# Kernel tuning notes

Measured on AMD Instinct MI355X. Metric: run time of the kernel, lower is better.

The kernel has to match this reference:

```python
import jax, jax.numpy as jnp
import numpy as np

B, S, T = 128, 512, 128
E, He, Ed, H = 512, 512, 512, 512


def setup_inputs() -> dict:
    key = jax.random.key(0)
    ks = jax.random.split(key, 13)
    w = lambda k, shape: jax.random.normal(k, shape, jnp.float32) * 0.02
    return {
        "trg_embed": jax.random.normal(ks[0], (B, T, E), jnp.float32),
        "edit_representation_final": jax.random.normal(ks[1], (1, B, 2 * Ed), jnp.float32),
        "edit_representation_cell_state": jax.random.normal(ks[2], (1, B, 2 * Ed), jnp.float32),
        "encoder_hidden": jax.random.normal(ks[3], (B, S, 2 * He), jnp.float32),
        "encoder_final": jax.random.normal(ks[4], (1, B, 2 * He), jnp.float32),
        "encoder_cell_state": jax.random.normal(ks[5], (1, B, 2 * He), jnp.float32),
        "src_mask": jnp.ones((B, 1, S), dtype=bool),
        "W_key": w(ks[6], (2 * He, H)),
        "W_query": w(ks[7], (H, H)),
        "w_energy": w(ks[8], (H,)),
        "W_bridge": w(ks[9], (2 * He + 2 * Ed, H)),
        "b_bridge": jnp.zeros((H,), jnp.float32),
        "W_ih": w(ks[10], (4 * H, E + 2 * He + 2 * Ed)),
        "W_hh": w(ks[11], (4 * H, H)),
        "b_ih": jnp.zeros((4 * H,), jnp.float32),
        "b_hh": jnp.zeros((4 * H,), jnp.float32),
        "W_pre": w(ks[12], (H, H + 2 * He + E)),
    }


def reference(trg_embed, edit_representation_final, edit_representation_cell_state,
              encoder_hidden, encoder_final, encoder_cell_state, src_mask,
              W_key, W_query, w_energy, W_bridge, b_bridge,
              W_ih, W_hh, b_ih, b_hh, W_pre):
    # bridge: init hidden / cell from final encoder + edit states  [1,B,H]
    h0 = jnp.tanh(jnp.concatenate([encoder_final, edit_representation_final], -1) @ W_bridge + b_bridge)
    c0 = jnp.tanh(jnp.concatenate([encoder_cell_state, edit_representation_cell_state], -1) @ W_bridge + b_bridge)
    proj_key = encoder_hidden @ W_key              # [B,S,H] (computed once)
    edit_flat = edit_representation_final[0]       # [B,2*Ed]
    mask = src_mask[:, 0, :]                       # [B,S]
    bias = b_ih + b_hh

    def step(carry, x_t):
        h, c = carry                               # [B,H] each
        # Bahdanau attention
        q = h @ W_query                            # [B,H]
        scores = jnp.tanh(q[:, None, :] + proj_key) @ w_energy   # [B,S]
        scores = jnp.where(mask, scores, -jnp.inf)
        alphas = jax.nn.softmax(scores, axis=-1)
        context = jnp.einsum('bs,bsd->bd', alphas, encoder_hidden)  # [B,2*He]
        # LSTM cell (torch gate order: i, f, g, o)
        rnn_in = jnp.concatenate([x_t, context, edit_flat], -1)
        gates = rnn_in @ W_ih.T + h @ W_hh.T + bias
        i_g, f_g, g_g, o_g = jnp.split(gates, 4, axis=-1)
        c_new = jax.nn.sigmoid(f_g) * c + jax.nn.sigmoid(i_g) * jnp.tanh(g_g)
        h_new = jax.nn.sigmoid(o_g) * jnp.tanh(c_new)
        # pre-output projection (dropout in eval mode = identity)
        pre = jnp.concatenate([x_t, h_new, context], -1) @ W_pre.T
        return (h_new, c_new), (h_new, pre)

    (h_last, c_last), (states, pre_outs) = jax.lax.scan(
        step, (h0[0], c0[0]), jnp.swapaxes(trg_embed, 0, 1))
    decoder_states = jnp.swapaxes(states, 0, 1)       # [B,T,H]
    pre_output_vectors = jnp.swapaxes(pre_outs, 0, 1) # [B,T,H]
    return decoder_states, h_last[None], pre_output_vectors
```

## Files before the change

### kernel.cpp

```cpp
#include <hip/hip_runtime.h>
#include <hip/hip_bf16.h>

typedef unsigned short u16;
typedef unsigned int u32;
typedef unsigned char u8;

typedef __attribute__((ext_vector_type(8))) __bf16 bf16x8;
typedef __attribute__((ext_vector_type(4))) float f32x4;
typedef __attribute__((ext_vector_type(2))) float f32x2;

__device__ __forceinline__ float fast_tanh(float x){
    float e = __expf(2.0f*x);
    return 1.0f - 2.0f/(e+1.0f);
}
__device__ __forceinline__ float fast_sigmoid(float x){
    return 1.0f/(1.0f+__expf(-x));
}
__device__ __forceinline__ float bflo(u32 u){ return __uint_as_float(u<<16); }
__device__ __forceinline__ float bfhi(u32 u){ return __uint_as_float(u & 0xffff0000u); }
__device__ __forceinline__ float bf2f(u16 u){ return __uint_as_float(((u32)u)<<16); }
__device__ __forceinline__ u16 f2bf(float v){
    __hip_bfloat16 h = __float2bfloat16(v);
    return *reinterpret_cast<u16*>(&h);
}
__device__ __forceinline__ f32x2 fp8lo(u32 u){ return __builtin_amdgcn_cvt_pk_f32_fp8(u, false); }
__device__ __forceinline__ f32x2 fp8hi(u32 u){ return __builtin_amdgcn_cvt_pk_f32_fp8(u, true); }

__device__ __forceinline__ void gridbar(int* bar, int e){
    __syncthreads();
    if (threadIdx.x == 0){
        const int g = blockIdx.x & 7;
        int* gcnt = bar + g*32;
        int* gall = bar + 256;
        int* gate = bar + 288;
        int prev = __hip_atomic_fetch_add(gcnt, 1, __ATOMIC_ACQ_REL, __HIP_MEMORY_SCOPE_AGENT);
        if (prev == e*32 - 1){
            int pg = __hip_atomic_fetch_add(gall, 1, __ATOMIC_ACQ_REL, __HIP_MEMORY_SCOPE_AGENT);
            if (pg == e*8 - 1)
                __hip_atomic_store(gate, e, __ATOMIC_RELEASE, __HIP_MEMORY_SCOPE_AGENT);
        }
        while (__hip_atomic_load(gate, __ATOMIC_RELAXED, __HIP_MEMORY_SCOPE_AGENT) < e)
            __builtin_amdgcn_s_sleep(4);
        (void)__hip_atomic_load(gate, __ATOMIC_ACQUIRE, __HIP_MEMORY_SCOPE_AGENT);
    }
    __syncthreads();
}

__device__ __forceinline__ void pairbar(int* pflags, int e){
    __syncthreads();
    if (threadIdx.x == 0){
        __hip_atomic_store(&pflags[blockIdx.x*32], e, __ATOMIC_RELEASE, __HIP_MEMORY_SCOPE_AGENT);
        int partner = (blockIdx.x ^ 1)*32;
        while (__hip_atomic_load(&pflags[partner], __ATOMIC_RELAXED, __HIP_MEMORY_SCOPE_AGENT) < e)
            __builtin_amdgcn_s_sleep(2);
        (void)__hip_atomic_load(&pflags[partner], __ATOMIC_ACQUIRE, __HIP_MEMORY_SCOPE_AGENT);
    }
    __syncthreads();
}

template<int C_MODE, int HAS_BIAS>
__global__ __launch_bounds__(256) void mfma_gemm(
    const u16* __restrict__ A, int lda,
    const u16* __restrict__ Bw, int ldb,
    const float* __restrict__ bias,
    void* __restrict__ Cp, long ldc, int K)
{
    __shared__ u16 Ash[128*64];
    __shared__ u16 Bsh[128*64];
    const int tid  = threadIdx.x;
    const int w    = tid >> 6;
    const int lane = tid & 63;
    const int wr   = w >> 1, wc = w & 1;
    const int row0 = blockIdx.y * 128, col0 = blockIdx.x * 128;

    f32x4 acc[4][4];
    #pragma unroll
    for (int i = 0; i < 4; i++)
        #pragma unroll
        for (int j = 0; j < 4; j++)
            acc[i][j] = f32x4{0.f,0.f,0.f,0.f};

    for (int k0 = 0; k0 < K; k0 += 64) {
        #pragma unroll
        for (int it = 0; it < 4; it++) {
            int j = it*256 + tid;
            int row = j >> 3, s = j & 7;
            const u16* src = A + (size_t)(row0 + row) * lda + k0 + ((s ^ (row & 7)) << 3);
            __builtin_amdgcn_global_load_lds(
                (const __attribute__((address_space(1))) unsigned int*)src,
                (__attribute__((address_space(3))) unsigned int*)(Ash + (size_t)(it*256 + w*64)*8),
                16, 0, 0);
        }
        #pragma unroll
        for (int it = 0; it < 4; it++) {
            int j = it*256 + tid;
            int row = j >> 3, s = j & 7;
            const u16* src = Bw + (size_t)(col0 + row) * ldb + k0 + ((s ^ (row & 7)) << 3);
            __builtin_amdgcn_global_load_lds(
                (const __attribute__((address_space(1))) unsigned int*)src,
                (__attribute__((address_space(3))) unsigned int*)(Bsh + (size_t)(it*256 + w*64)*8),
                16, 0, 0);
        }
        __syncthreads();
        #pragma unroll
        for (int kh = 0; kh < 2; kh++) {
            bf16x8 af[4], bg[4];
            #pragma unroll
            for (int f = 0; f < 4; f++) {
                int row = wr*64 + f*16 + (lane & 15);
                int slot = (kh*4 + (lane >> 4)) ^ (row & 7);
                af[f] = *(const bf16x8*)(Ash + row*64 + slot*8);
                int nn = wc*64 + f*16 + (lane & 15);
                int slot2 = (kh*4 + (lane >> 4)) ^ (nn & 7);
                bg[f] = *(const bf16x8*)(Bsh + nn*64 + slot2*8);
            }
            #pragma unroll
            for (int fm = 0; fm < 4; fm++)
                #pragma unroll
                for (int fn = 0; fn < 4; fn++)
                    acc[fm][fn] = __builtin_amdgcn_mfma_f32_16x16x32_bf16(af[fm], bg[fn], acc[fm][fn], 0, 0, 0);
        }
        __syncthreads();
    }

    #pragma unroll
    for (int fm = 0; fm < 4; fm++) {
        #pragma unroll
        for (int fn = 0; fn < 4; fn++) {
            int col = col0 + wc*64 + fn*16 + (lane & 15);
            #pragma unroll
            for (int r = 0; r < 4; r++) {
                int row = row0 + wr*64 + fm*16 + ((lane >> 4)<<2) + r;
                float v = acc[fm][fn][r];
                if (HAS_BIAS) v += bias[col];
                if (C_MODE == 1)
                    ((u16*)Cp)[(size_t)row * ldc + col] = f2bf(v);
                else
                    ((float*)Cp)[(((size_t)(row & 127)) << 16) + ((size_t)(row >> 7) << 9) + col] = v;
            }
        }
    }
}

__global__ __launch_bounds__(1024, 4) void k_mega(
    u16* __restrict__ pre_in,
    const u16* __restrict__ Wq_t,
    const u8*  __restrict__ pk8,
    const float* __restrict__ we_g,
    const u8*  __restrict__ enc8,
    const u16* __restrict__ Wg,
    const u16* __restrict__ edit_part,
    u16* __restrict__ gates_part,
    float* __restrict__ scores_g,
    u16* __restrict__ h_glob,
    float* __restrict__ cbuf,
    float* __restrict__ out_states,
    float* __restrict__ out_hlast,
    int* __restrict__ bar)
{
    __shared__ __align__(16) u8 pk_lds[131072];
    __shared__ __align__(16) u8 scr[24576];
    __shared__ float hs[512];
    __shared__ float qf[544];
    __shared__ float al[512];
    float* qp   = (float*)scr;
    float* red  = (float*)scr;
    float* spp  = (float*)scr;
    float* cp8  = (float*)scr;
    float* fold = (float*)(scr + 18432);
    u16* Ash = (u16*)scr;
    u16* Bsh = (u16*)(scr + 16384);
    int* pflags = bar + 320;
    const int bid = blockIdx.x, tid = threadIdx.x;
    const int w = tid >> 6, lane = tid & 63;
    const int b = bid >> 1, half = bid & 1;

    {
        const u8* srcb = pk8 + ((size_t)(b*512 + half*256))*512;
        #pragma unroll
        for (int i = 0; i < 8; i++)
            __builtin_amdgcn_global_load_lds(
                (const __attribute__((address_space(1))) unsigned int*)(srcb + i*16384 + tid*16),
                (__attribute__((address_space(3))) unsigned int*)(pk_lds + i*16384 + (size_t)w*1024),
                16, 0, 0);
    }
    float wel[16];
    {
        const int l = lane & 31;
        #pragma unroll
        for (int i = 0; i < 16; i++) wel[i] = we_g[l*16 + i];
    }
    asm volatile("s_waitcnt vmcnt(0)" ::: "memory");
    __syncthreads();

    for (int t = 0; t < 129; t++) {
        if (t == 0) {
            if (tid < 512) hs[tid] = bf2f(h_glob[b*512 + tid]);
        } else if (tid < 512) {
            const int j = tid;
            float g4[4];
            #pragma unroll
            for (int g = 0; g < 4; g++) {
                float s = bf2f(edit_part[b*2048 + g*512 + j]);
                #pragma unroll
                for (int kk = 0; kk < 8; kk++)
                    s += bf2f(gates_part[(size_t)kk*262144 + b*2048 + g*512 + j]);
                g4[g] = s;
            }
            float c  = cbuf[(size_t)(t & 1)*65536 + b*512 + j];
            float cn = fast_sigmoid(g4[1])*c + fast_sigmoid(g4[0])*fast_tanh(g4[2]);
            float hn = fast_sigmoid(g4[3])*fast_tanh(cn);
            cbuf[(size_t)((t+1) & 1)*65536 + b*512 + j] = cn;
            hs[j] = hn;
            u16 hb = f2bf(hn);
            h_glob[b*512 + j] = hb;
            pre_in[(size_t)(t-1)*262144 + b*2048 + 1536 + j] = hb;
            out_states[(size_t)b*65536 + (size_t)(t-1)*512 + j] = hn;
            if (t == 128) out_hlast[b*512 + j] = hn;
        }
        if (t == 128) break;
        __syncthreads();
        {
            const int j = tid & 511, kh3 = tid >> 9;
            const uint4* row = (const uint4*)(Wq_t + (size_t)j*512 + (size_t)kh3*256);
            float a = 0.f;
            #pragma unroll 8
            for (int c8 = 0; c8 < 32; c8++) {
                uint4 u = row[c8];
                int k = kh3*256 + c8*8;
                a += hs[k+0]*bflo(u.x) + hs[k+1]*bfhi(u.x)
                   + hs[k+2]*bflo(u.y) + hs[k+3]*bfhi(u.y)
                   + hs[k+4]*bflo(u.z) + hs[k+5]*bfhi(u.z)
                   + hs[k+6]*bflo(u.w) + hs[k+7]*bfhi(u.w);
            }
            qp[tid] = a;
        }
        __syncthreads();
        if (tid < 512) qf[tid + (tid >> 4)] = qp[tid] + qp[512 + tid];
        __syncthreads();
        {
            float ql[16];
            const int l = lane & 31;
            #pragma unroll
            for (int i = 0; i < 16; i++) ql[i] = qf[l*17 + i];
            #pragma unroll
            for (int it = 0; it < 8; it++) {
                const int s = it*32 + w*2 + (lane >> 5);
                const uint4 u = *(const uint4*)(pk_lds + (size_t)s*512 + l*16);
                float a2 = 0.f;
                f32x2 p;
                p = fp8lo(u.x); a2 += fast_tanh(ql[0]+p.x)*wel[0] + fast_tanh(ql[1]+p.y)*wel[1];
                p = fp8hi(u.x); a2 += fast_tanh(ql[2]+p.x)*wel[2] + fast_tanh(ql[3]+p.y)*wel[3];
                p = fp8lo(u.y); a2 += fast_tanh(ql[4]+p.x)*wel[4] + fast_tanh(ql[5]+p.y)*wel[5];
                p = fp8hi(u.y); a2 += fast_tanh(ql[6]+p.x)*wel[6] + fast_tanh(ql[7]+p.y)*wel[7];
                p = fp8lo(u.z); a2 += fast_tanh(ql[8]+p.x)*wel[8] + fast_tanh(ql[9]+p.y)*wel[9];
                p = fp8hi(u.z); a2 += fast_tanh(ql[10]+p.x)*wel[10] + fast_tanh(ql[11]+p.y)*wel[11];
                p = fp8lo(u.w); a2 += fast_tanh(ql[12]+p.x)*wel[12] + fast_tanh(ql[13]+p.y)*wel[13];
                p = fp8hi(u.w); a2 += fast_tanh(ql[14]+p.x)*wel[14] + fast_tanh(ql[15]+p.y)*wel[15];
                #pragma unroll
                for (int o = 16; o; o >>= 1) a2 += __shfl_xor(a2, o);
                if (l == 0) spp[s] = a2;
            }
        }
        __syncthreads();
        if (tid < 256) scores_g[b*512 + half*256 + tid] = spp[tid];
        pairbar(pflags, t + 1);

        {
            const int s = tid & 511;
            float sc = scores_g[b*512 + s];
            float m = sc;
            #pragma unroll
            for (int o = 32; o; o >>= 1) m = fmaxf(m, __shfl_xor(m, o));
            if (lane == 0) red[w] = m;
            __syncthreads();
            m = red[0];
            #pragma unroll
            for (int i = 1; i < 16; i++) m = fmaxf(m, red[i]);
            float p = __expf(sc - m);
            float sm = p;
            #pragma unroll
            for (int o = 32; o; o >>= 1) sm += __shfl_xor(sm, o);
            if (lane == 0) red[16 + w] = sm;
            __syncthreads();
            sm = red[16];
            #pragma unroll
            for (int i = 17; i < 24; i++) sm += red[i];
            al[s] = p * (1.f / sm);
        }
        __syncthreads();
        {
            const int ch = tid & 31, sg = tid >> 5;
            const uint4* eb = (const uint4*)(enc8 + (size_t)b*524288 + (size_t)half*512 + (size_t)ch*16);
            float c[16];
            #pragma unroll
            for (int e = 0; e < 16; e++) c[e] = 0.f;
            #pragma unroll 4
            for (int s2 = 0; s2 < 16; s2++) {
                int s = sg*16 + s2;
                uint4 u = eb[(size_t)s*64];
                float a = al[s];
                f32x2 p;
                p = fp8lo(u.x); c[0] += a*p.x; c[1] += a*p.y;
                p = fp8hi(u.x); c[2] += a*p.x; c[3] += a*p.y;
                p = fp8lo(u.y); c[4] += a*p.x; c[5] += a*p.y;
                p = fp8hi(u.y); c[6] += a*p.x; c[7] += a*p.y;
                p = fp8lo(u.z); c[8] += a*p.x; c[9] += a*p.y;
                p = fp8hi(u.z); c[10]+= a*p.x; c[11]+= a*p.y;
                p = fp8lo(u.w); c[12]+= a*p.x; c[13]+= a*p.y;
                p = fp8hi(u.w); c[14]+= a*p.x; c[15]+= a*p.y;
            }
            #pragma unroll
            for (int e = 0; e < 16; e++) c[e] += __shfl_xor(c[e], 32);
            #pragma unroll
            for (int p2 = 0; p2 < 2; p2++) {
                if (lane < 32) {
                    #pragma unroll
                    for (int e = 0; e < 8; e++)
                        cp8[(w*32 + ch)*9 + e] = c[p2*8 + e];
                }
                __syncthreads();
                if (tid < 256) {
                    const int ch2 = tid >> 3, e2 = tid & 7;
                    float v = 0.f;
                    #pragma unroll
                    for (int g = 0; g < 16; g++) v += cp8[(g*32 + ch2)*9 + e2];
                    fold[ch2*16 + p2*8 + e2] = v;
                }
                __syncthreads();
            }
        }
        if (tid < 256) {
            u32 pack = (u32)f2bf(fold[2*tid]) | ((u32)f2bf(fold[2*tid+1]) << 16);
            *(u32*)&pre_in[(size_t)t*262144 + b*2048 + 512 + half*512 + 2*tid] = pack;
        }
        gridbar(bar, 2*t + 1);

        {
            const int cb = bid & 31, ks = bid >> 5;
            const int col0 = cb*64;
            const int wrC = w >> 2, wcC = w & 3;
            const u16* prow_t = pre_in + (size_t)t*262144;
            f32x4 acc[2];
            acc[0] = f32x4{0.f,0.f,0.f,0.f};
            acc[1] = f32x4{0.f,0.f,0.f,0.f};
            const int rowA = tid >> 3, slA = tid & 7;
            const int gkA = (slA ^ (rowA & 7)) << 3;
            const int rowB = (tid & 511) >> 3;
            const int gkB = ((tid & 7) ^ (rowB & 7)) << 3;
            #pragma unroll
            for (int kt = 0; kt < 4; kt++) {
                const int k0 = ks*256 + kt*64;
                {
                    const u16* srcA = (ks < 6)
                        ? prow_t + (size_t)rowA*2048 + k0 + gkA
                        : h_glob + (size_t)rowA*512 + (k0 - 1536) + gkA;
                    __builtin_amdgcn_global_load_lds(
                        (const __attribute__((address_space(1))) unsigned int*)srcA,
                        (__attribute__((address_space(3))) unsigned int*)(Ash + (size_t)w*512),
                        16, 0, 0);
                }
                if (tid < 512) {
                    const u16* srcB = Wg + (size_t)(col0 + rowB)*2048 + k0 + gkB;
                    __builtin_amdgcn_global_load_lds(
                        (const __attribute__((address_space(1))) unsigned int*)srcB,
                        (__attribute__((address_space(3))) unsigned int*)(Bsh + (size_t)w*512),
                        16, 0, 0);
                }
                __syncthreads();
                #pragma unroll
                for (int kh = 0; kh < 2; kh++) {
                    bf16x8 bg;
                    {
                        int nn = wcC*16 + (lane & 15);
                        int slot2 = (kh*4 + (lane >> 4)) ^ (nn & 7);
                        bg = *(const bf16x8*)(Bsh + nn*64 + slot2*8);
                    }
                    #pragma unroll
                    for (int f = 0; f < 2; f++) {
                        int row = wrC*32 + f*16 + (lane & 15);
                        int slot = (kh*4 + (lane >> 4)) ^ (row & 7);
                        bf16x8 af = *(const bf16x8*)(Ash + row*64 + slot*8);
                        acc[f] = __builtin_amdgcn_mfma_f32_16x16x32_bf16(af, bg, acc[f], 0, 0, 0);
                    }
                }
                __syncthreads();
            }
            u16* gp = gates_part + (size_t)ks*262144;
            #pragma unroll
            for (int f = 0; f < 2; f++) {
                int cl = col0 + wcC*16 + (lane & 15);
                #pragma unroll
                for (int r = 0; r < 4; r++) {
                    int bb = wrC*32 + f*16 + ((lane >> 4) << 2) + r;
                    gp[(size_t)bb*2048 + cl] = f2bf(acc[f][r]);
                }
            }
        }
        gridbar(bar, 2*t + 2);
    }
}

__global__ __launch_bounds__(256) void k_cvt_bf16(const float4* __restrict__ in, ushort4* __restrict__ out, int n4){
    int i = blockIdx.x*256 + threadIdx.x;
    if (i >= n4) return;
    float4 v = in[i];
    ushort4 o;
    o.x = f2bf(v.x); o.y = f2bf(v.y); o.z = f2bf(v.z); o.w = f2bf(v.w);
    out[i] = o;
}

__global__ __launch_bounds__(256) void k_cvt_fp8_f32(const float4* __restrict__ in, uint2* __restrict__ out, int n8){
    int i = blockIdx.x*256 + threadIdx.x;
    if (i >= n8) return;
    float4 v0 = in[2*i], v1 = in[2*i+1];
    u32 lo = 0, hi = 0;
    lo = __builtin_amdgcn_cvt_pk_fp8_f32(v0.x, v0.y, lo, false);
    lo = __builtin_amdgcn_cvt_pk_fp8_f32(v0.z, v0.w, lo, true);
    hi = __builtin_amdgcn_cvt_pk_fp8_f32(v1.x, v1.y, hi, false);
    hi = __builtin_amdgcn_cvt_pk_fp8_f32(v1.z, v1.w, hi, true);
    out[i] = make_uint2(lo, hi);
}

__global__ __launch_bounds__(256) void k_cvt_fp8_bf16(const uint4* __restrict__ in, uint2* __restrict__ out, int n8){
    int i = blockIdx.x*256 + threadIdx.x;
    if (i >= n8) return;
    uint4 u = in[i];
    u32 lo = 0, hi = 0;
    lo = __builtin_amdgcn_cvt_pk_fp8_f32(bflo(u.x), bfhi(u.x), lo, false);
    lo = __builtin_amdgcn_cvt_pk_fp8_f32(bflo(u.y), bfhi(u.y), lo, true);
    hi = __builtin_amdgcn_cvt_pk_fp8_f32(bflo(u.z), bfhi(u.z), hi, false);
    hi = __builtin_amdgcn_cvt_pk_fp8_f32(bflo(u.w), bfhi(u.w), hi, true);
    out[i] = make_uint2(lo, hi);
}

__global__ __launch_bounds__(256) void k_bias(const float* __restrict__ a, const float* __restrict__ b, float* __restrict__ o){
    int i = blockIdx.x*256 + threadIdx.x;
    o[i] = a[i] + b[i];
}

__global__ __launch_bounds__(256) void k_cvt_slice(
    u16* __restrict__ out, const float* __restrict__ in,
    int kshift, int ldi, int koff, int ldo, int obase)
{
    int i = blockIdx.x*256 + threadIdx.x;
    int n = i >> kshift, k = i & ((1 << kshift) - 1);
    out[(size_t)n*ldo + obase + k] = f2bf(in[(size_t)n*ldi + koff + k]);
}

__global__ __launch_bounds__(256) void k_tr_bf16(u16* __restrict__ out, const float* __restrict__ in, int K, int N){
    __shared__ float t[32][33];
    int k0 = blockIdx.x*32, n0 = blockIdx.y*32;
    int tx = threadIdx.x & 31, ty = threadIdx.x >> 5;
    for (int i = ty; i < 32; i += 8)
        t[i][tx] = in[(size_t)(k0+i)*N + n0 + tx];
    __syncthreads();
    for (int i = ty; i < 32; i += 8)
        out[(size_t)(n0+i)*K + k0 + tx] = f2bf(t[tx][i]);
}

__global__ __launch_bounds__(256) void k_build_prex(const float4* __restrict__ trg4, u16* __restrict__ pre_in){
    int i = blockIdx.x*256 + threadIdx.x;
    float4 v = trg4[i];
    int kq = i & 127, tt = (i >> 7) & 127, bb = i >> 14;
    ushort4 o;
    o.x = f2bf(v.x); o.y = f2bf(v.y); o.z = f2bf(v.z); o.w = f2bf(v.w);
    *(ushort4*)&pre_in[((size_t)tt*128 + bb)*2048 + kq*4] = o;
}

__global__ __launch_bounds__(256) void k_bridge(
    const float* __restrict__ encf, const float* __restrict__ editf,
    const float* __restrict__ encc, const float* __restrict__ editc,
    const float* __restrict__ Wb, const float* __restrict__ bb,
    u16* __restrict__ h_glob, float* __restrict__ cbuf)
{
    int tid = blockIdx.x*256 + threadIdx.x;
    int sel = tid >> 16;
    int rem = tid & 65535;
    int b = rem >> 9, j = rem & 511;
    const float* s1 = sel ? encc : encf;
    const float* s2 = sel ? editc : editf;
    float acc = bb[j];
    for (int k = 0; k < 1024; k++) acc += s1[b*1024+k] * Wb[k*512 + j];
    for (int k = 0; k < 1024; k++) acc += s2[b*1024+k] * Wb[(1024+k)*512 + j];
    float v = fast_tanh(acc);
    if (sel) cbuf[65536 + rem] = v;
    else     h_glob[rem] = f2bf(v);
}

extern "C" void kernel_launch(void* const* d_in, const int* in_sizes, int n_in,
                              void* d_out, int out_size, void* d_ws, size_t ws_size,
                              hipStream_t stream)
{
    const float* trg      = (const float*)d_in[0];
    const float* editf    = (const float*)d_in[1];
    const float* editc    = (const float*)d_in[2];
    const float* enc      = (const float*)d_in[3];
    const float* encf     = (const float*)d_in[4];
    const float* encc     = (const float*)d_in[5];
    const float* W_key    = (const float*)d_in[7];
    const float* W_query  = (const float*)d_in[8];
    const float* w_energy = (const float*)d_in[9];
    const float* W_bridge = (const float*)d_in[10];
    const float* b_bridge = (const float*)d_in[11];
    const float* W_ih     = (const float*)d_in[12];
    const float* W_hh     = (const float*)d_in[13];
    const float* b_ih     = (const float*)d_in[14];
    const float* b_hh     = (const float*)d_in[15];
    const float* W_pre    = (const float*)d_in[16];
    (void)in_sizes; (void)n_in; (void)out_size; (void)ws_size;

    char* ws = (char*)d_ws;
    size_t off = 0;
    auto alloc = [&](size_t bytes)->char* {
        char* p = ws + off;
        off = (off + bytes + 255) & ~(size_t)255;
        return p;
    };

    u16* enc_b      = (u16*)alloc((size_t)67108864*2);
    u16* pk_b       = (u16*)alloc((size_t)33554432*2);
    u8*  enc8       = (u8*) alloc((size_t)67108864);
    u8*  pk8        = (u8*) alloc((size_t)33554432);
    u16* pre_in     = (u16*)alloc((size_t)33554432*2);
    u16* edit_b     = (u16*)alloc((size_t)131072*2);
    u16* edit_part  = (u16*)alloc((size_t)262144*2);
    u16* Wgfull     = (u16*)alloc((size_t)4194304*2);
    u16* Wedit      = (u16*)alloc((size_t)2097152*2);
    u16* Wp_all     = (u16*)alloc((size_t)1048576*2);
    u16* Wq_t       = (u16*)alloc((size_t)262144*2);
    u16* Wk_t       = (u16*)alloc((size_t)524288*2);
    u16* h_glob     = (u16*)alloc((size_t)65536*2);
    float* cbuf       = (float*)alloc((size_t)131072*4);
    float* bias_comb  = (float*)alloc((size_t)2048*4);
    float* scores_g   = (float*)alloc((size_t)65536*4);
    u16*   gates_part = (u16*)alloc((size_t)2097152*2);
    int*   bar        = (int*)alloc((size_t)(320 + 256*32)*4);

    hipMemsetAsync(bar, 0, (size_t)(320 + 256*32)*4, stream);

    k_cvt_bf16<<<65536, 256, 0, stream>>>((const float4*)enc,   (ushort4*)enc_b,  16777216);
    k_cvt_fp8_f32<<<32768, 256, 0, stream>>>((const float4*)enc, (uint2*)enc8, 8388608);
    k_cvt_bf16<<<128,   256, 0, stream>>>((const float4*)editf, (ushort4*)edit_b, 32768);
    k_bias<<<8, 256, 0, stream>>>(b_ih, b_hh, bias_comb);

    k_cvt_slice<<<4096, 256, 0, stream>>>(Wgfull, W_ih,  9,  2560, 0,    2048, 0);
    k_cvt_slice<<<8192, 256, 0, stream>>>(Wgfull, W_ih,  10, 2560, 512,  2048, 512);
    k_cvt_slice<<<4096, 256, 0, stream>>>(Wgfull, W_hh,  9,  512,  0,    2048, 1536);
    k_cvt_slice<<<8192, 256, 0, stream>>>(Wedit,  W_ih,  10, 2560, 1536, 1024, 0);
    k_cvt_slice<<<1024, 256, 0, stream>>>(Wp_all, W_pre, 9,  2048, 0,    2048, 0);
    k_cvt_slice<<<2048, 256, 0, stream>>>(Wp_all, W_pre, 10, 2048, 1024, 2048, 512);
    k_cvt_slice<<<1024, 256, 0, stream>>>(Wp_all, W_pre, 9,  2048, 512,  2048, 1536);
    k_tr_bf16<<<dim3(16,16), 256, 0, stream>>>(Wq_t, W_query, 512, 512);
    k_tr_bf16<<<dim3(32,16), 256, 0, stream>>>(Wk_t, W_key, 1024, 512);

    k_build_prex<<<8192, 256, 0, stream>>>((const float4*)trg, pre_in);

    mfma_gemm<1,1><<<dim3(16,1), 256, 0, stream>>>(edit_b, 1024, Wedit, 1024,
        bias_comb, edit_part, 2048, 1024);
    mfma_gemm<1,0><<<dim3(4,512), 256, 0, stream>>>(enc_b, 1024, Wk_t, 1024,
        nullptr, pk_b, 512, 1024);
    k_cvt_fp8_bf16<<<16384, 256, 0, stream>>>((const uint4*)pk_b, (uint2*)pk8, 4194304);

    k_bridge<<<512, 256, 0, stream>>>(encf, editf, encc, editc, W_bridge, b_bridge, h_glob, cbuf);

    float* out_states = (float*)d_out;
    float* out_hlast  = (float*)d_out + 8388608;
    float* out_pre    = (float*)d_out + 8454144;

    k_mega<<<256, 1024, 0, stream>>>(pre_in, Wq_t, pk8, w_energy, enc8, Wgfull,
        edit_part, gates_part, scores_g, h_glob, cbuf, out_states, out_hlast, bar);

    mfma_gemm<2,0><<<dim3(4,128), 256, 0, stream>>>(pre_in, 2048, Wp_all, 2048,
        nullptr, out_pre, 0, 2048);
}
```

Measured before the change: 12.35 ms.

## Double-buffer encoder context loads into LDS via async global_load_lds

The attention-context reduction now streams the fp8 encoder rows into two LDS buffers with global_load_lds, prefetching the next 16-row chunk while the current one is accumulated. Each wave handles one source row per chunk, and the cross-wave fold is reworked for the new 8-element-per-lane layout. This targets the latency of direct global loads in the context loop. In exchange it adds 64 block-wide barriers per timestep, uses a serialized 32-iteration loop, and issues the first prefetch before the softmax.

Measured after the change: 20.79 ms. +68.4%, slower.

```diff
diff --git a/kernel.cpp b/kernel.cpp
--- a/kernel.cpp
+++ b/kernel.cpp
@@ -166,8 +166,10 @@
     float* qp   = (float*)scr;
     float* red  = (float*)scr;
     float* spp  = (float*)scr;
-    float* cp8  = (float*)scr;
-    float* fold = (float*)(scr + 18432);
+    u8* ebuf0 = scr + 2048;
+    u8* ebuf1 = scr + 10240;
+    float* cpB  = (float*)scr;
+    float* foldB= (float*)(scr + 20480);
     u16* Ash = (u16*)scr;
     u16* Bsh = (u16*)(scr + 16384);
     int* pflags = bar + 320;
@@ -192,6 +194,8 @@
     }
     asm volatile("s_waitcnt vmcnt(0)" ::: "memory");
     __syncthreads();
+
+    const u8* encb = enc8 + (size_t)b*524288 + (size_t)half*512;
 
     for (int t = 0; t < 129; t++) {
         if (t == 0) {
@@ -266,6 +270,12 @@
         if (tid < 256) scores_g[b*512 + half*256 + tid] = spp[tid];
         pairbar(pflags, t + 1);
 
+        if (tid < 512) {
+            __builtin_amdgcn_global_load_lds(
+                (const __attribute__((address_space(1))) unsigned int*)(encb + (size_t)(tid >> 5)*1024 + (size_t)(tid & 31)*16),
+                (__attribute__((address_space(3))) unsigned int*)(ebuf0 + (size_t)w*1024),
+                16, 0, 0);
+        }
         {
             const int s = tid & 511;
             float sc = scores_g[b*512 + s];
@@ -290,48 +300,54 @@
         }
         __syncthreads();
         {
-            const int ch = tid & 31, sg = tid >> 5;
-            const uint4* eb = (const uint4*)(enc8 + (size_t)b*524288 + (size_t)half*512 + (size_t)ch*16);
-            float c[16];
-            #pragma unroll
-            for (int e = 0; e < 16; e++) c[e] = 0.f;
-            #pragma unroll 4
-            for (int s2 = 0; s2 < 16; s2++) {
-                int s = sg*16 + s2;
-                uint4 u = eb[(size_t)s*64];
-                float a = al[s];
-                f32x2 p;
-                p = fp8lo(u.x); c[0] += a*p.x; c[1] += a*p.y;
-                p = fp8hi(u.x); c[2] += a*p.x; c[3] += a*p.y;
-                p = fp8lo(u.y); c[4] += a*p.x; c[5] += a*p.y;
-                p = fp8hi(u.y); c[6] += a*p.x; c[7] += a*p.y;
-                p = fp8lo(u.z); c[8] += a*p.x; c[9] += a*p.y;
-                p = fp8hi(u.z); c[10]+= a*p.x; c[11]+= a*p.y;
-                p = fp8lo(u.w); c[12]+= a*p.x; c[13]+= a*p.y;
-                p = fp8hi(u.w); c[14]+= a*p.x; c[15]+= a*p.y;
-            }
-            #pragma unroll
-            for (int e = 0; e < 16; e++) c[e] += __shfl_xor(c[e], 32);
+            float cacc[8];
+            #pragma unroll
+            for (int e = 0; e < 8; e++) cacc[e] = 0.f;
+            for (int c = 0; c < 32; c++) {
+                const u8* cur = (c & 1) ? ebuf1 : ebuf0;
+                u8* nxt = (c & 1) ? ebuf0 : ebuf1;
+                if (c + 1 < 32) {
+                    if (tid < 512) {
+                        __builtin_amdgcn_global_load_lds(
+                            (const __attribute__((address_space(1))) unsigned int*)(encb + (size_t)(c+1)*16384 + (size_t)(tid >> 5)*1024 + (size_t)(tid & 31)*16),
+                            (__attribute__((address_space(3))) unsigned int*)(nxt + (size_t)w*1024),
+                            16, 0, 0);
+                    }
+                    asm volatile("s_waitcnt vmcnt(1)" ::: "memory");
+                } else {
+                    asm volatile("s_waitcnt vmcnt(0)" ::: "memory");
+                }
+                __syncthreads();
+                {
+                    float a = al[c*16 + w];
+                    uint2 u = *(const uint2*)(cur + (size_t)w*512 + (size_t)lane*8);
+                    f32x2 p;
+                    p = fp8lo(u.x); cacc[0] += a*p.x; cacc[1] += a*p.y;
+                    p = fp8hi(u.x); cacc[2] += a*p.x; cacc[3] += a*p.y;
+                    p = fp8lo(u.y); cacc[4] += a*p.x; cacc[5] += a*p.y;
+                    p = fp8hi(u.y); cacc[6] += a*p.x; cacc[7] += a*p.y;
+                }
+                __syncthreads();
+            }
             #pragma unroll
             for (int p2 = 0; p2 < 2; p2++) {
-                if (lane < 32) {
-                    #pragma unroll
-                    for (int e = 0; e < 8; e++)
-                        cp8[(w*32 + ch)*9 + e] = c[p2*8 + e];
-                }
+                #pragma unroll
+                for (int e = 0; e < 4; e++)
+                    cpB[(w*64 + lane)*5 + e] = cacc[p2*4 + e];
                 __syncthreads();
                 if (tid < 256) {
-                    const int ch2 = tid >> 3, e2 = tid & 7;
+                    const int col8 = tid >> 2, eo = tid & 3;
                     float v = 0.f;
                     #pragma unroll
-                    for (int g = 0; g < 16; g++) v += cp8[(g*32 + ch2)*9 + e2];
-                    fold[ch2*16 + p2*8 + e2] = v;
+                    for (int ww = 0; ww < 16; ww++)
+                        v += cpB[(ww*64 + col8)*5 + eo];
+                    foldB[col8*8 + p2*4 + eo] = v;
                 }
                 __syncthreads();
             }
         }
         if (tid < 256) {
-            u32 pack = (u32)f2bf(fold[2*tid]) | ((u32)f2bf(fold[2*tid+1]) << 16);
+            u32 pack = (u32)f2bf(foldB[2*tid]) | ((u32)f2bf(foldB[2*tid+1]) << 16);
             *(u32*)&pre_in[(size_t)t*262144 + b*2048 + 512 + half*512 + 2*tid] = pack;
         }
         gridbar(bar, 2*t + 1);
```
